# Performance work log

Hardware: AMD Instinct MI355X
Metric: run time of the kernel (lower is better)

The kernel has to match this reference:

```python
import jax, jax.numpy as jnp
import numpy as np

B, S_LEN, H_LEN, DIM = 2048, 64, 256, 256
NULL_ATT = -float(2 ** 22)


def setup_inputs() -> dict:
    key = jax.random.key(0)
    k1, k2, k3, k4, k5, k6, k7 = jax.random.split(key, 7)
    return {
        "item_emb": jax.random.normal(k1, (B, DIM), dtype=jnp.float32),
        "x_session": jax.random.normal(k2, (B, S_LEN, DIM), dtype=jnp.float32),
        "session_len": jax.random.randint(k3, (B,), 0, S_LEN, dtype=jnp.int32),
        "user_hist": jax.random.normal(k4, (B, H_LEN, DIM), dtype=jnp.float32),
        "hist_len": jax.random.randint(k5, (B,), 0, H_LEN, dtype=jnp.int32),
        "W1": jax.random.normal(k6, (DIM, 2 * DIM), dtype=jnp.float32) * 0.05,
        "b1": jax.random.normal(k7, (DIM,), dtype=jnp.float32) * 0.05,
    }


def reference(item_emb, x_session, session_len, user_hist, hist_len, W1, b1):
    # item_emb [B,d], x_session [B,s,d], user_hist [B,h,d]
    batch, s_len, dim = x_session.shape
    h_len = user_hist.shape[1]
    # fc1 query does not depend on history position -> compute once per (b,s)
    q_in = jnp.concatenate(
        [jnp.broadcast_to(item_emb[:, None, :], x_session.shape), x_session], axis=-1
    )  # [B,s,2d]
    query = q_in @ W1.T + b1  # [B,s,d]
    # attention scores: sum over dim of hist * query for every (s,h) pair
    att = jnp.einsum("bsd,bhd->bsh", query, user_hist)  # [B,s,h]
    mask_s = (jnp.arange(s_len)[None, :] < session_len[:, None])[:, :, None]
    mask_h = (jnp.arange(h_len)[None, :] < hist_len[:, None])[:, None, :]
    att = jnp.where(mask_s & mask_h, att, jnp.float32(NULL_ATT))
    score = jnp.max(att, axis=1)  # max over session positions -> [B,h]
    w = jax.nn.softmax(score, axis=1)  # [B,h]
    user_hist_rep = jnp.sum(user_hist * w[:, :, None], axis=1)  # [B,d]
    return user_hist_rep, score
```

## Files before the change

kernel.cpp:

```cpp
#include <hip/hip_runtime.h>

#define NB 2048
#define NULL_ATT (-4194304.0f)

typedef __attribute__((ext_vector_type(8))) _Float16 f16x8;
typedef __attribute__((ext_vector_type(2))) _Float16 h2;
typedef __attribute__((ext_vector_type(4))) float f32x4;

__device__ __align__(16) short g_wxf16[256 * 256];
__device__ float g_iq[NB * 256];

__device__ __forceinline__ int qoff(int s, int k) {
    int g = k >> 3;
    return s * 256 + (((g ^ (s & 7)) << 3) | (k & 7));
}

__device__ __forceinline__ f16x8 cvt8h(float4 a, float4 b) {
    f16x8 r;
    r[0] = (_Float16)a.x; r[1] = (_Float16)a.y; r[2] = (_Float16)a.z; r[3] = (_Float16)a.w;
    r[4] = (_Float16)b.x; r[5] = (_Float16)b.y; r[6] = (_Float16)b.z; r[7] = (_Float16)b.w;
    return r;
}

__device__ __forceinline__ void issue16(const float* __restrict__ p, float4 r[8][2]) {
    #pragma unroll
    for (int kc = 0; kc < 8; ++kc) {
        r[kc][0] = *(const float4*)(p + kc * 32);
        r[kc][1] = *(const float4*)(p + kc * 32 + 4);
    }
}
__device__ __forceinline__ void conv16(const float4 r[8][2], f16x8 dst[8]) {
    #pragma unroll
    for (int kc = 0; kc < 8; ++kc) dst[kc] = cvt8h(r[kc][0], r[kc][1]);
}

__global__ __launch_bounds__(256, 2) void prep(const float* __restrict__ item_emb,
                                               const float* __restrict__ W1,
                                               const float* __restrict__ b1) {
    if (blockIdx.x < 256) {
        int j = blockIdx.x, k = threadIdx.x;
        g_wxf16[j * 256 + k] =
            __builtin_bit_cast(short, (_Float16)W1[(size_t)j * 512 + 256 + k]);
        return;
    }
    const int m0 = (blockIdx.x - 256) * 16;
    const int t = threadIdx.x, wave = t >> 6, lane = t & 63;
    const int lr = lane & 15, lo8 = lane >> 4;
    const int jb = wave * 64;

    float4 ir[8][2];
    issue16(item_emb + (size_t)(m0 + lr) * 256 + lo8 * 8, ir);
    f16x8 afr[8];
    conv16(ir, afr);

    f32x4 acc[4];
    #pragma unroll
    for (int jt = 0; jt < 4; ++jt) acc[jt] = f32x4{0.f, 0.f, 0.f, 0.f};
    #pragma unroll
    for (int kc = 0; kc < 8; ++kc) {
        #pragma unroll
        for (int jt = 0; jt < 4; ++jt) {
            const float* wp = W1 + (size_t)(jb + jt * 16 + lr) * 512 + kc * 32 + lo8 * 8;
            f16x8 bfr = cvt8h(*(const float4*)wp, *(const float4*)(wp + 4));
            acc[jt] = __builtin_amdgcn_mfma_f32_16x16x32_f16(afr[kc], bfr, acc[jt], 0, 0, 0);
        }
    }
    #pragma unroll
    for (int jt = 0; jt < 4; ++jt) {
        float bv = b1[jb + jt * 16 + lr];
        #pragma unroll
        for (int i = 0; i < 4; ++i)
            g_iq[(size_t)(m0 + lo8 * 4 + i) * 256 + jb + jt * 16 + lr] = acc[jt][i] + bv;
    }
}

#define AA_GET(i) (h2{parr[(i) >> 2][(((i) & 3) << 1)], parr[(i) >> 2][(((i) & 3) << 1) | 1]})
#define AA_SET(i, v) { parr[(i) >> 2][(((i) & 3) << 1)] = (v)[0]; \
                       parr[(i) >> 2][(((i) & 3) << 1) | 1] = (v)[1]; }

__global__ __launch_bounds__(256, 2) void coatt_main(
    const float* __restrict__ x_session,
    const int*   __restrict__ session_len,
    const float* __restrict__ user_hist,
    const int*   __restrict__ hist_len,
    float* __restrict__ out)
{
    const int b = blockIdx.x;
    const int t = threadIdx.x;
    const int wave = t >> 6;
    const int lane = t & 63;
    const int lr  = lane & 15;
    const int lo8 = lane >> 4;
    const int sl = session_len[b];
    const int hl = hist_len[b];

    __shared__ __align__(16) short qf[64 * 256];
    __shared__ float sMax[256];
    __shared__ float red2[8];
    __shared__ __align__(16) float Vp[4][256];

    sMax[t] = NULL_ATT;
    const int nst = (sl > 0) ? min(4, (sl + 15) >> 4) : 0;
    const int nht = (hl + 15) >> 4;
    const bool p2 = (nst > 0 && hl > 0);
    const float* hB = user_hist + (size_t)b * 256 * 256;
    const bool havePre = p2 && (wave < nht);

    float4 hraw[8][2];
    f16x8 bcur[8];

    if (wave < nst) {
        const int st = wave;
        float4 xraw[8][2];
        issue16(x_session + ((size_t)b * 64 + st * 16 + lr) * 256 + lo8 * 8, xraw);
        if (havePre)
            issue16(hB + (size_t)(wave * 16 + lr) * 256 + lo8 * 8, hraw);
        f16x8 afr[8];
        conv16(xraw, afr);

        #pragma unroll
        for (int jc = 0; jc < 4; ++jc) {
            f32x4 acc[4];
            #pragma unroll
            for (int jt = 0; jt < 4; ++jt) {
                float v = g_iq[(size_t)b * 256 + jc * 64 + jt * 16 + lr];
                acc[jt] = f32x4{v, v, v, v};
            }
            #pragma unroll
            for (int kc = 0; kc < 8; ++kc) {
                #pragma unroll
                for (int jt = 0; jt < 4; ++jt) {
                    f16x8 bfr2 = *(const f16x8*)&g_wxf16[(jc * 64 + jt * 16 + lr) * 256 + kc * 32 + lo8 * 8];
                    acc[jt] = __builtin_amdgcn_mfma_f32_16x16x32_f16(afr[kc], bfr2, acc[jt], 0, 0, 0);
                }
            }
            #pragma unroll
            for (int jt = 0; jt < 4; ++jt) {
                int j = jc * 64 + jt * 16 + lr;
                #pragma unroll
                for (int i = 0; i < 4; ++i)
                    qf[qoff(st * 16 + lo8 * 4 + i, j)] =
                        __builtin_bit_cast(short, (_Float16)acc[jt][i]);
            }
        }
    } else if (havePre) {
        issue16(hB + (size_t)(wave * 16 + lr) * 256 + lo8 * 8, hraw);
    }
    if (havePre) conv16(hraw, bcur);
    __syncthreads();

    float Mrun = -3.0e38f;
    float Drun = 0.0f;
    f16x8 parr[8];
    #pragma unroll
    for (int kc = 0; kc < 8; ++kc) parr[kc] = f16x8{0, 0, 0, 0, 0, 0, 0, 0};

    if (p2) {
        for (int slot = 0; slot < 4; ++slot) {
            const int ht = wave + slot * 4;
            if (ht >= nht) break;
            const int htn = ht + 4;
            const bool pre = (htn < nht);
            if (pre)
                issue16(hB + (size_t)(htn * 16 + lr) * 256 + lo8 * 8, hraw);

            f32x4 acc[4];
            #pragma unroll
            for (int st = 0; st < 4; ++st) acc[st] = f32x4{0.f, 0.f, 0.f, 0.f};
            #pragma unroll
            for (int kc = 0; kc < 8; ++kc) {
                #pragma unroll
                for (int st = 0; st < 4; ++st) {
                    if (st < nst) {
                        f16x8 a = *(const f16x8*)&qf[qoff(st * 16 + lr, kc * 32 + lo8 * 8)];
                        acc[st] = __builtin_amdgcn_mfma_f32_16x16x32_f16(a, bcur[kc], acc[st], 0, 0, 0);
                    }
                }
            }
            float m = NULL_ATT;
            #pragma unroll
            for (int st = 0; st < 4; ++st) {
                if (st < nst) {
                    #pragma unroll
                    for (int i = 0; i < 4; ++i) {
                        int s = st * 16 + lo8 * 4 + i;
                        if (s < sl) m = fmaxf(m, acc[st][i]);
                    }
                }
            }
            m = fmaxf(m, __shfl_xor(m, 16, 64));
            m = fmaxf(m, __shfl_xor(m, 32, 64));
            const int h = ht * 16 + lr;
            if (lane < 16 && h < hl) sMax[h] = m;

            float sh = (h < hl) ? m : NULL_ATT;
            float mt = sh;
            mt = fmaxf(mt, __shfl_xor(mt, 1, 64));
            mt = fmaxf(mt, __shfl_xor(mt, 2, 64));
            mt = fmaxf(mt, __shfl_xor(mt, 4, 64));
            mt = fmaxf(mt, __shfl_xor(mt, 8, 64));
            if (mt > Mrun) {
                float scl = __expf(Mrun - mt);
                Drun *= scl;
                const _Float16 s16 = (_Float16)scl;
                f16x8 s8 = {s16, s16, s16, s16, s16, s16, s16, s16};
                #pragma unroll
                for (int kc = 0; kc < 8; ++kc) parr[kc] *= s8;
                Mrun = mt;
            }
            float eh = __expf(sh - Mrun);
            Drun += eh;

            {
                const _Float16 e16 = (_Float16)eh;
                f16x8 e8 = {e16, e16, e16, e16, e16, e16, e16, e16};
                #pragma unroll
                for (int kc = 0; kc < 8; ++kc) parr[kc] = bcur[kc] * e8 + parr[kc];
            }
            if (pre) conv16(hraw, bcur);
        }

        #pragma unroll
        for (int sb = 0; sb < 4; ++sb) {
            const int bmask = 8 >> sb;
            const int half = 16 >> sb;
            const bool hi = (lr & bmask) != 0;
            #pragma unroll
            for (int i = 0; i < (16 >> sb); ++i) {
                h2 a0 = AA_GET(i);
                h2 a1 = AA_GET(i + half);
                h2 keep = hi ? a1 : a0;
                h2 send = hi ? a0 : a1;
                int ru = __shfl_xor(__builtin_bit_cast(int, send), bmask, 64);
                h2 res = keep + __builtin_bit_cast(h2, ru);
                AA_SET(i, res);
            }
        }
        h2 f0 = AA_GET(0), f1 = AA_GET(1);

        float Dl = Drun;
        Dl += __shfl_xor(Dl, 1, 64);
        Dl += __shfl_xor(Dl, 2, 64);
        Dl += __shfl_xor(Dl, 4, 64);
        Dl += __shfl_xor(Dl, 8, 64);
        if (lane == 0) { red2[wave] = Mrun; red2[4 + wave] = Dl; }
        const int col0 = (lr >> 1) * 32 + lo8 * 8 + (lr & 1) * 4;
        *(float4*)&Vp[wave][col0] =
            float4{(float)f0[0], (float)f0[1], (float)f1[0], (float)f1[1]};
    }
    __syncthreads();

    float sc = sMax[t];
    out[(size_t)NB * 256 + (size_t)b * 256 + t] = sc;

    if (p2) {
        float M0 = red2[0], M1 = red2[1], M2 = red2[2], M3 = red2[3];
        float Ms = fmaxf(fmaxf(M0, M1), fmaxf(M2, M3));
        float w0 = __expf(M0 - Ms), w1 = __expf(M1 - Ms);
        float w2 = __expf(M2 - Ms), w3 = __expf(M3 - Ms);
        float denom = w0 * red2[4] + w1 * red2[5] + w2 * red2[6] + w3 * red2[7];
        float num = w0 * Vp[0][t] + w1 * Vp[1][t] + w2 * Vp[2][t] + w3 * Vp[3][t];
        out[(size_t)b * 256 + t] = num / denom;
    } else {
        f32x4 a4 = {0.f, 0.f, 0.f, 0.f};
        const float* hc = hB + lane * 4;
        for (int h = wave; h < 256; h += 16) {
            float4 v0 = *(const float4*)(hc + (size_t)(h)      * 256);
            float4 v1 = *(const float4*)(hc + (size_t)(h + 4)  * 256);
            float4 v2 = *(const float4*)(hc + (size_t)(h + 8)  * 256);
            float4 v3 = *(const float4*)(hc + (size_t)(h + 12) * 256);
            a4[0] += (v0.x + v1.x) + (v2.x + v3.x);
            a4[1] += (v0.y + v1.y) + (v2.y + v3.y);
            a4[2] += (v0.z + v1.z) + (v2.z + v3.z);
            a4[3] += (v0.w + v1.w) + (v2.w + v3.w);
        }
        *(float4*)&Vp[wave][lane * 4] = float4{a4[0], a4[1], a4[2], a4[3]};
        __syncthreads();
        out[(size_t)b * 256 + t] =
            ((Vp[0][t] + Vp[1][t]) + (Vp[2][t] + Vp[3][t])) * (1.0f / 256.0f);
    }
}

extern "C" void kernel_launch(void* const* d_in, const int* in_sizes, int n_in,
                              void* d_out, int out_size, void* d_ws, size_t ws_size,
                              hipStream_t stream) {
    const float* item_emb    = (const float*)d_in[0];
    const float* x_session   = (const float*)d_in[1];
    const int*   session_len = (const int*)d_in[2];
    const float* user_hist   = (const float*)d_in[3];
    const int*   hist_len    = (const int*)d_in[4];
    const float* W1          = (const float*)d_in[5];
    const float* b1          = (const float*)d_in[6];
    float* out = (float*)d_out;

    prep<<<384, 256, 0, stream>>>(item_emb, W1, b1);
    coatt_main<<<NB, 256, 0, stream>>>(x_session, session_len, user_hist, hist_len, out);
}
```

Measured before the change: 163.9 us.

## Split query GEMM into separate kernel writing fp16 queries to global memory

The per-batch query projection moves out of the main attention kernel into its own qgemm kernel, which writes fp16 query tiles to a workspace buffer, with a static global fallback if the workspace is too small. The main kernel drops its 32 KB of shared-memory query staging and reads the query fragments straight from global memory. This lowers LDS use in the main kernel so more blocks can be resident, and removes the prologue that stalled history loads. In exchange it adds a launch plus a write and re-read of about 8 MB of query data through global memory and cache.

```diff
diff --git a/kernel.cpp b/kernel.cpp
--- a/kernel.cpp
+++ b/kernel.cpp
@@ -9,11 +9,7 @@
 
 __device__ __align__(16) short g_wxf16[256 * 256];
 __device__ float g_iq[NB * 256];
-
-__device__ __forceinline__ int qoff(int s, int k) {
-    int g = k >> 3;
-    return s * 256 + (((g ^ (s & 7)) << 3) | (k & 7));
-}
+__device__ __align__(16) short g_qfallback[NB * 64 * 256];
 
 __device__ __forceinline__ f16x8 cvt8h(float4 a, float4 b) {
     f16x8 r;
@@ -74,12 +70,57 @@
     }
 }
 
+__global__ __launch_bounds__(256, 2) void qgemm(const float* __restrict__ x_session,
+                                                const int* __restrict__ session_len,
+                                                short* __restrict__ qb) {
+    const int b = blockIdx.x;
+    const int t = threadIdx.x, wave = t >> 6, lane = t & 63;
+    const int lr = lane & 15, lo8 = lane >> 4;
+    const int sl = session_len[b];
+    const int nst = (sl > 0) ? min(4, (sl + 15) >> 4) : 0;
+    if (wave >= nst) return;
+
+    const int st = wave;
+    float4 xraw[8][2];
+    issue16(x_session + ((size_t)b * 64 + st * 16 + lr) * 256 + lo8 * 8, xraw);
+    f16x8 afr[8];
+    conv16(xraw, afr);
+
+    #pragma unroll
+    for (int jc = 0; jc < 4; ++jc) {
+        f32x4 acc[4];
+        #pragma unroll
+        for (int jt = 0; jt < 4; ++jt) {
+            float v = g_iq[(size_t)b * 256 + jc * 64 + jt * 16 + lr];
+            acc[jt] = f32x4{v, v, v, v};
+        }
+        #pragma unroll
+        for (int kc = 0; kc < 8; ++kc) {
+            #pragma unroll
+            for (int jt = 0; jt < 4; ++jt) {
+                f16x8 bfr2 = *(const f16x8*)&g_wxf16[(jc * 64 + jt * 16 + lr) * 256 + kc * 32 + lo8 * 8];
+                acc[jt] = __builtin_amdgcn_mfma_f32_16x16x32_f16(afr[kc], bfr2, acc[jt], 0, 0, 0);
+            }
+        }
+        #pragma unroll
+        for (int jt = 0; jt < 4; ++jt) {
+            const int j = jc * 64 + jt * 16 + lr;
+            #pragma unroll
+            for (int i = 0; i < 4; ++i) {
+                const int s = st * 16 + lo8 * 4 + i;
+                qb[((size_t)b * 64 + s) * 256 + j] =
+                    __builtin_bit_cast(short, (_Float16)acc[jt][i]);
+            }
+        }
+    }
+}
+
 #define AA_GET(i) (h2{parr[(i) >> 2][(((i) & 3) << 1)], parr[(i) >> 2][(((i) & 3) << 1) | 1]})
 #define AA_SET(i, v) { parr[(i) >> 2][(((i) & 3) << 1)] = (v)[0]; \
                        parr[(i) >> 2][(((i) & 3) << 1) | 1] = (v)[1]; }
 
 __global__ __launch_bounds__(256, 2) void coatt_main(
-    const float* __restrict__ x_session,
+    const short* __restrict__ qb,
     const int*   __restrict__ session_len,
     const float* __restrict__ user_hist,
     const int*   __restrict__ hist_len,
@@ -94,7 +135,6 @@
     const int sl = session_len[b];
     const int hl = hist_len[b];
 
-    __shared__ __align__(16) short qf[64 * 256];
     __shared__ float sMax[256];
     __shared__ float red2[8];
     __shared__ __align__(16) float Vp[4][256];
@@ -104,50 +144,7 @@
     const int nht = (hl + 15) >> 4;
     const bool p2 = (nst > 0 && hl > 0);
     const float* hB = user_hist + (size_t)b * 256 * 256;
-    const bool havePre = p2 && (wave < nht);
-
-    float4 hraw[8][2];
-    f16x8 bcur[8];
-
-    if (wave < nst) {
-        const int st = wave;
-        float4 xraw[8][2];
-        issue16(x_session + ((size_t)b * 64 + st * 16 + lr) * 256 + lo8 * 8, xraw);
-        if (havePre)
-            issue16(hB + (size_t)(wave * 16 + lr) * 256 + lo8 * 8, hraw);
-        f16x8 afr[8];
-        conv16(xraw, afr);
-
-        #pragma unroll
-        for (int jc = 0; jc < 4; ++jc) {
-            f32x4 acc[4];
-            #pragma unroll
-            for (int jt = 0; jt < 4; ++jt) {
-                float v = g_iq[(size_t)b * 256 + jc * 64 + jt * 16 + lr];
-                acc[jt] = f32x4{v, v, v, v};
-            }
-            #pragma unroll
-            for (int kc = 0; kc < 8; ++kc) {
-                #pragma unroll
-                for (int jt = 0; jt < 4; ++jt) {
-                    f16x8 bfr2 = *(const f16x8*)&g_wxf16[(jc * 64 + jt * 16 + lr) * 256 + kc * 32 + lo8 * 8];
-                    acc[jt] = __builtin_amdgcn_mfma_f32_16x16x32_f16(afr[kc], bfr2, acc[jt], 0, 0, 0);
-                }
-            }
-            #pragma unroll
-            for (int jt = 0; jt < 4; ++jt) {
-                int j = jc * 64 + jt * 16 + lr;
-                #pragma unroll
-                for (int i = 0; i < 4; ++i)
-                    qf[qoff(st * 16 + lo8 * 4 + i, j)] =
-                        __builtin_bit_cast(short, (_Float16)acc[jt][i]);
-            }
-        }
-    } else if (havePre) {
-        issue16(hB + (size_t)(wave * 16 + lr) * 256 + lo8 * 8, hraw);
-    }
-    if (havePre) conv16(hraw, bcur);
-    __syncthreads();
+    const short* qT = qb + (size_t)b * 64 * 256;
 
     float Mrun = -3.0e38f;
     float Drun = 0.0f;
@@ -156,6 +153,12 @@
     for (int kc = 0; kc < 8; ++kc) parr[kc] = f16x8{0, 0, 0, 0, 0, 0, 0, 0};
 
     if (p2) {
+        float4 hraw[8][2];
+        f16x8 bcur[8];
+        if (wave < nht) {
+            issue16(hB + (size_t)(wave * 16 + lr) * 256 + lo8 * 8, hraw);
+            conv16(hraw, bcur);
+        }
         for (int slot = 0; slot < 4; ++slot) {
             const int ht = wave + slot * 4;
             if (ht >= nht) break;
@@ -172,7 +175,7 @@
                 #pragma unroll
                 for (int st = 0; st < 4; ++st) {
                     if (st < nst) {
-                        f16x8 a = *(const f16x8*)&qf[qoff(st * 16 + lr, kc * 32 + lo8 * 8)];
+                        f16x8 a = *(const f16x8*)&qT[(st * 16 + lr) * 256 + kc * 32 + lo8 * 8];
                         acc[st] = __builtin_amdgcn_mfma_f32_16x16x32_f16(a, bcur[kc], acc[st], 0, 0, 0);
                     }
                 }
@@ -293,6 +296,17 @@
     const float* b1          = (const float*)d_in[6];
     float* out = (float*)d_out;
 
+    const size_t qbytes = (size_t)NB * 64 * 256 * sizeof(short);
+    short* qbuf;
+    if (ws_size >= qbytes) {
+        qbuf = (short*)d_ws;
+    } else {
+        void* p;
+        hipGetSymbolAddress(&p, HIP_SYMBOL(g_qfallback));
+        qbuf = (short*)p;
+    }
+
     prep<<<384, 256, 0, stream>>>(item_emb, W1, b1);
-    coatt_main<<<NB, 256, 0, stream>>>(x_session, session_len, user_hist, hist_len, out);
-}
+    qgemm<<<NB, 256, 0, stream>>>(x_session, session_len, qbuf);
+    coatt_main<<<NB, 256, 0, stream>>>(qbuf, session_len, user_hist, hist_len, out);
+}
```

Measured after the change: 264.0 us. 1.61x slower.

## Double block size to eight waves splitting query projection and history tiles

Applied to the files above, without the earlier changes.

Raises coatt_main from 256 to 512 threads (8 waves). The query projection is split across wave pairs by output-column half, and the history tiles are spread over 8 waves, two slots each. The softmax merge and the fallback path are generalized to combine 8 partial results. The intent is more latency hiding and shorter per-wave serial work per batch row. The cost is higher register and LDS pressure per block, with launch_bounds(512,2) possibly forcing register spills.

```diff
diff --git a/kernel.cpp b/kernel.cpp
--- a/kernel.cpp
+++ b/kernel.cpp
@@ -78,7 +78,7 @@
 #define AA_SET(i, v) { parr[(i) >> 2][(((i) & 3) << 1)] = (v)[0]; \
                        parr[(i) >> 2][(((i) & 3) << 1) | 1] = (v)[1]; }
 
-__global__ __launch_bounds__(256, 2) void coatt_main(
+__global__ __launch_bounds__(512, 2) void coatt_main(
     const float* __restrict__ x_session,
     const int*   __restrict__ session_len,
     const float* __restrict__ user_hist,
@@ -96,10 +96,10 @@
 
     __shared__ __align__(16) short qf[64 * 256];
     __shared__ float sMax[256];
-    __shared__ float red2[8];
-    __shared__ __align__(16) float Vp[4][256];
-
-    sMax[t] = NULL_ATT;
+    __shared__ float red2[16];
+    __shared__ __align__(16) float Vp[8][256];
+
+    if (t < 256) sMax[t] = NULL_ATT;
     const int nst = (sl > 0) ? min(4, (sl + 15) >> 4) : 0;
     const int nht = (hl + 15) >> 4;
     const bool p2 = (nst > 0 && hl > 0);
@@ -109,8 +109,9 @@
     float4 hraw[8][2];
     f16x8 bcur[8];
 
-    if (wave < nst) {
-        const int st = wave;
+    if ((wave & 3) < nst) {
+        const int st = wave & 3;
+        const int jh = wave >> 2;
         float4 xraw[8][2];
         issue16(x_session + ((size_t)b * 64 + st * 16 + lr) * 256 + lo8 * 8, xraw);
         if (havePre)
@@ -119,7 +120,8 @@
         conv16(xraw, afr);
 
         #pragma unroll
-        for (int jc = 0; jc < 4; ++jc) {
+        for (int jc2 = 0; jc2 < 2; ++jc2) {
+            const int jc = jh * 2 + jc2;
             f32x4 acc[4];
             #pragma unroll
             for (int jt = 0; jt < 4; ++jt) {
@@ -156,10 +158,11 @@
     for (int kc = 0; kc < 8; ++kc) parr[kc] = f16x8{0, 0, 0, 0, 0, 0, 0, 0};
 
     if (p2) {
-        for (int slot = 0; slot < 4; ++slot) {
-            const int ht = wave + slot * 4;
+        #pragma unroll
+        for (int slot = 0; slot < 2; ++slot) {
+            const int ht = wave + slot * 8;
             if (ht >= nht) break;
-            const int htn = ht + 4;
+            const int htn = ht + 8;
             const bool pre = (htn < nht);
             if (pre)
                 issue16(hB + (size_t)(htn * 16 + lr) * 256 + lo8 * 8, hraw);
@@ -243,41 +246,41 @@
         Dl += __shfl_xor(Dl, 2, 64);
         Dl += __shfl_xor(Dl, 4, 64);
         Dl += __shfl_xor(Dl, 8, 64);
-        if (lane == 0) { red2[wave] = Mrun; red2[4 + wave] = Dl; }
+        if (lane == 0) { red2[wave] = Mrun; red2[8 + wave] = Dl; }
         const int col0 = (lr >> 1) * 32 + lo8 * 8 + (lr & 1) * 4;
         *(float4*)&Vp[wave][col0] =
             float4{(float)f0[0], (float)f0[1], (float)f1[0], (float)f1[1]};
-    }
-    __syncthreads();
-
-    float sc = sMax[t];
-    out[(size_t)NB * 256 + (size_t)b * 256 + t] = sc;
-
-    if (p2) {
-        float M0 = red2[0], M1 = red2[1], M2 = red2[2], M3 = red2[3];
-        float Ms = fmaxf(fmaxf(M0, M1), fmaxf(M2, M3));
-        float w0 = __expf(M0 - Ms), w1 = __expf(M1 - Ms);
-        float w2 = __expf(M2 - Ms), w3 = __expf(M3 - Ms);
-        float denom = w0 * red2[4] + w1 * red2[5] + w2 * red2[6] + w3 * red2[7];
-        float num = w0 * Vp[0][t] + w1 * Vp[1][t] + w2 * Vp[2][t] + w3 * Vp[3][t];
-        out[(size_t)b * 256 + t] = num / denom;
     } else {
         f32x4 a4 = {0.f, 0.f, 0.f, 0.f};
         const float* hc = hB + lane * 4;
-        for (int h = wave; h < 256; h += 16) {
+        for (int h = wave; h < 256; h += 32) {
             float4 v0 = *(const float4*)(hc + (size_t)(h)      * 256);
-            float4 v1 = *(const float4*)(hc + (size_t)(h + 4)  * 256);
-            float4 v2 = *(const float4*)(hc + (size_t)(h + 8)  * 256);
-            float4 v3 = *(const float4*)(hc + (size_t)(h + 12) * 256);
+            float4 v1 = *(const float4*)(hc + (size_t)(h + 8)  * 256);
+            float4 v2 = *(const float4*)(hc + (size_t)(h + 16) * 256);
+            float4 v3 = *(const float4*)(hc + (size_t)(h + 24) * 256);
             a4[0] += (v0.x + v1.x) + (v2.x + v3.x);
             a4[1] += (v0.y + v1.y) + (v2.y + v3.y);
             a4[2] += (v0.z + v1.z) + (v2.z + v3.z);
             a4[3] += (v0.w + v1.w) + (v2.w + v3.w);
         }
         *(float4*)&Vp[wave][lane * 4] = float4{a4[0], a4[1], a4[2], a4[3]};
-        __syncthreads();
-        out[(size_t)b * 256 + t] =
-            ((Vp[0][t] + Vp[1][t]) + (Vp[2][t] + Vp[3][t])) * (1.0f / 256.0f);
+        if (lane == 0) { red2[wave] = 0.f; red2[8 + wave] = 32.f; }
+    }
+    __syncthreads();
+
+    if (t < 256) {
+        out[(size_t)NB * 256 + (size_t)b * 256 + t] = sMax[t];
+        float Ms = red2[0];
+        #pragma unroll
+        for (int w = 1; w < 8; ++w) Ms = fmaxf(Ms, red2[w]);
+        float num = 0.f, den = 0.f;
+        #pragma unroll
+        for (int w = 0; w < 8; ++w) {
+            float ww = __expf(red2[w] - Ms);
+            den += ww * red2[8 + w];
+            num += ww * Vp[w][t];
+        }
+        out[(size_t)b * 256 + t] = num / den;
     }
 }
 
@@ -294,5 +297,5 @@
     float* out = (float*)d_out;
 
     prep<<<384, 256, 0, stream>>>(item_emb, W1, b1);
-    coatt_main<<<NB, 256, 0, stream>>>(x_session, session_len, user_hist, hist_len, out);
-}
+    coatt_main<<<NB, 512, 0, stream>>>(x_session, session_len, user_hist, hist_len, out);
+}
```

New measurement: 205.6 us. +25.5%, slower.
